# Optimization experiments

Measured on AMD Instinct MI355X. Metric: run time of the kernel, lower is better.

Reference implementation:

```python
import jax, jax.numpy as jnp
import numpy as np

N = 20000      # points
K = 16         # neighbor pairs per query per branch
M = N * K      # total pairs
C = 384        # embed_dim
H = 6          # num_heads
HD = C // H    # head_dim = 64
H1 = H // 2    # cartesian-branch heads
L = 24         # quant_grid_length (window 6.0 / quant 0.25)
Q = 0.25       # quant_size
LS = 24        # quant_grid_length_sphere (120 / 5)
QS = 5.0       # quant_size_sphere
A = 0.05 * 0.25  # exponential_split 'a'
SCALE = HD ** -0.5


def setup_inputs() -> dict:
    key = jax.random.key(0)
    ks = jax.random.split(key, 12)
    s = 0.02
    inp = {}
    inp["query_feats"] = jax.random.normal(ks[0], (N, C), jnp.float32)
    inp["xyz"] = jax.random.uniform(ks[1], (N, 3), jnp.float32, -3.0, 3.0)
    inp["index_0"] = jnp.repeat(jnp.arange(N, dtype=jnp.int32), K)
    inp["index_1"] = jax.random.randint(ks[2], (M,), 0, N, dtype=jnp.int32)
    inp["index_0_sphere"] = jnp.repeat(jnp.arange(N, dtype=jnp.int32), K)
    inp["index_1_sphere"] = jax.random.randint(ks[3], (M,), 0, N, dtype=jnp.int32)
    inp["W_qkv"] = jax.random.normal(ks[4], (C, 3 * C), jnp.float32) * s
    inp["b_qkv"] = jnp.zeros((3 * C,), jnp.float32)
    inp["W_proj"] = jax.random.normal(ks[5], (C, C), jnp.float32) * s
    inp["b_proj"] = jnp.zeros((C,), jnp.float32)
    inp["tq"] = jax.random.normal(ks[6], (2 * L - 1, 3, H1, HD), jnp.float32) * s
    inp["tk"] = jax.random.normal(ks[7], (2 * L - 1, 3, H1, HD), jnp.float32) * s
    inp["tv"] = jax.random.normal(ks[8], (2 * L - 1, 3, H1, HD), jnp.float32) * s
    inp["tq_s"] = jax.random.normal(ks[9], (2 * LS, 3, H - H1, HD), jnp.float32) * s
    inp["tk_s"] = jax.random.normal(ks[10], (2 * LS, 3, H - H1, HD), jnp.float32) * s
    inp["tv_s"] = jax.random.normal(ks[11], (2 * LS, 3, H - H1, HD), jnp.float32) * s
    return inp


def _cart2sphere(xyz):
    x, y, z = xyz[:, 0], xyz[:, 1], xyz[:, 2]
    theta = (jnp.arctan2(y, x) + np.pi) * (180.0 / np.pi)
    beta = jnp.arctan2(jnp.sqrt(x * x + y * y), z) * (180.0 / np.pi)
    r = jnp.sqrt(x * x + y * y + z * z)
    return jnp.stack([theta, beta, r], -1)


def _rel_idx_cart(xyz, i0, i1):
    rel = xyz[i0] - xyz[i1]  # [M,3]
    idx = jnp.floor(rel / Q).astype(jnp.int32) + (L - 1)
    return jnp.clip(idx, 0, 2 * L - 2)


def _rel_idx_sphere(sph, i0, i1):
    rel = sph[i0] - sph[i1]  # [M,3] (theta, beta, r)
    idx01 = jnp.clip(jnp.floor(rel[:, :2] / QS).astype(jnp.int32) + LS, 0, 2 * LS - 1)
    # exponential_split on radial dim
    r = rel[:, 2]
    ra = jnp.abs(r)
    flag = (r >= 0).astype(jnp.float32)
    idx = 2.0 * jnp.floor(jnp.log((ra + 2.0 * A) / A) / np.log(2.0)) - 2.0
    idx = idx + ((3.0 * jnp.exp2(jnp.floor(idx / 2.0)) - 2.0) * A <= ra).astype(jnp.float32)
    idx = idx * (2.0 * flag - 1.0) + (flag - 1.0)
    idx2 = jnp.clip(idx.astype(jnp.int32) + 24, 0, 2 * LS - 1)
    return jnp.concatenate([idx01, idx2[:, None]], 1)


def _branch(q, k, v, i0, i1, rel_idx, Tq, Tk, Tv):
    # q,k,v: [N,h,d]; i0/i1: [M]; rel_idx: [M,3]; tables: [R,3,h,d]
    qg = q[i0]  # [M,h,d]
    kg = k[i1]
    attn = jnp.einsum('mhd,mhd->mh', qg, kg)
    for dim in range(3):
        attn = attn + jnp.einsum('mhd,mhd->mh', qg, Tq[rel_idx[:, dim], dim])
        attn = attn + jnp.einsum('mhd,mhd->mh', kg, Tk[rel_idx[:, dim], dim])
    # segment softmax over queries (i0)
    seg_max = jax.ops.segment_max(attn, i0, num_segments=N)
    ex = jnp.exp(attn - seg_max[i0])
    p = ex / jax.ops.segment_sum(ex, i0, num_segments=N)[i0]  # [M,h]
    vg = v[i1] + Tv[rel_idx[:, 0], 0] + Tv[rel_idx[:, 1], 1] + Tv[rel_idx[:, 2], 2]
    return jax.ops.segment_sum(p[:, :, None] * vg, i0, num_segments=N)  # [N,h,d]


def reference(query_feats, xyz, index_0, index_1, index_0_sphere, index_1_sphere,
              W_qkv, b_qkv, W_proj, b_proj, tq, tk, tv, tq_s, tk_s, tv_s):
    i0 = index_0.astype(jnp.int32)
    i1 = index_1.astype(jnp.int32)
    i0s = index_0_sphere.astype(jnp.int32)
    i1s = index_1_sphere.astype(jnp.int32)
    qkv = (query_feats @ W_qkv + b_qkv).reshape(N, 3, H, HD)
    q = qkv[:, 0] * SCALE
    k = qkv[:, 1]
    v = qkv[:, 2]
    sph = _cart2sphere(xyz)
    ri = _rel_idx_cart(xyz, i0, i1)
    out1 = _branch(q[:, :H1], k[:, :H1], v[:, :H1], i0, i1, ri, tq, tk, tv)
    ri_s = _rel_idx_sphere(sph, i0s, i1s)
    out2 = _branch(q[:, H1:], k[:, H1:], v[:, H1:], i0s, i1s, ri_s, tq_s, tk_s, tv_s)
    x = jnp.concatenate([out1, out2], 1).reshape(N, C)
    return x @ W_proj + b_proj
```

## Files before the change

kernel.cpp:

```cpp
#include <hip/hip_runtime.h>
#include <hip/hip_bf16.h>

namespace {

constexpr int NP   = 20000;
constexpr int CD   = 384;
constexpr int QKVD = 1152;
constexpr int TC   = 47 * 3 * 3 * 64;
constexpr int TS   = 48 * 3 * 3 * 64;

constexpr int PB0 = NP * CD / 4 / 256;
constexpr int PB1 = PB0 + (QKVD / 32) * (CD / 32);
constexpr int PB2 = PB1 + (CD / 32) * (CD / 32);
constexpr int PB3 = PB2 + 27 * 7;

typedef __attribute__((ext_vector_type(8))) short short8;
typedef __attribute__((ext_vector_type(4))) float f32x4;
typedef __attribute__((ext_vector_type(2))) float f32x2;

__device__ inline float f32_atan2(float y, float x) {
  return (float)atan2((double)y, (double)x);
}
__device__ inline float f32_log(float x) {
  return (float)log((double)x);
}

__device__ inline float bfl(unsigned u) {
  union { unsigned u; float f; } c; c.u = u << 16; return c.f;
}
__device__ inline float bfh(unsigned u) {
  union { unsigned u; float f; } c; c.u = u & 0xffff0000u; return c.f;
}
__device__ inline f32x2 up2(unsigned u) {
  f32x2 r;
  r.x = bfl(u);
  r.y = bfh(u);
  return r;
}
__device__ inline unsigned short f2bf(float x) {
  __hip_bfloat16 hb = __float2bfloat16(x);
  unsigned short u; __builtin_memcpy(&u, &hb, 2);
  return u;
}

#if __has_builtin(__builtin_amdgcn_fdot2_f32_bf16)
#define HAVE_BF16_DOT 1
typedef __attribute__((ext_vector_type(2))) __bf16 bf16x2_t;
__device__ inline float dot2bf(unsigned a, unsigned b, float c) {
  bf16x2_t av, bv;
  __builtin_memcpy(&av, &a, 4);
  __builtin_memcpy(&bv, &b, 4);
  return __builtin_amdgcn_fdot2_f32_bf16(av, bv, c, false);
}
#endif

__device__ inline void async16(const void* g, void* l) {
  __builtin_amdgcn_global_load_lds(
      (const __attribute__((address_space(1))) unsigned int*)g,
      (__attribute__((address_space(3))) unsigned int*)l,
      16, 0, 0);
}

__global__ __launch_bounds__(256) void prep_all_k(const float* __restrict__ qf,
                                                  unsigned short* __restrict__ qf_b,
                                                  const float* __restrict__ Wqkv,
                                                  unsigned short* __restrict__ wqkvT,
                                                  const float* __restrict__ Wproj,
                                                  unsigned short* __restrict__ wprojT,
                                                  const float* __restrict__ tq,
                                                  const float* __restrict__ tk,
                                                  const float* __restrict__ tv,
                                                  const float* __restrict__ tqs,
                                                  const float* __restrict__ tks,
                                                  const float* __restrict__ tvs,
                                                  unsigned short* __restrict__ tq_b,
                                                  unsigned short* __restrict__ tk_b,
                                                  unsigned short* __restrict__ tv_b,
                                                  unsigned short* __restrict__ tqs_b,
                                                  unsigned short* __restrict__ tks_b,
                                                  unsigned short* __restrict__ tvs_b,
                                                  const float* __restrict__ xyz,
                                                  float* __restrict__ sph) {
  const int bid = blockIdx.x;
  const int tid = threadIdx.x;
  __shared__ float t[32][33];

  if (bid < PB0) {
    int i = (bid * 256 + tid) * 4;
    float4 v = *(const float4*)(qf + i);
    ushort4 o;
    o.x = f2bf(v.x); o.y = f2bf(v.y); o.z = f2bf(v.z); o.w = f2bf(v.w);
    *(ushort4*)(qf_b + i) = o;
  } else if (bid < PB2) {
    const float* in;
    unsigned short* out;
    int R, Cc, bx, by;
    if (bid < PB1) {
      in = Wqkv; out = wqkvT; R = CD; Cc = QKVD;
      int tt = bid - PB0; bx = tt % (QKVD / 32); by = tt / (QKVD / 32);
    } else {
      in = Wproj; out = wprojT; R = CD; Cc = CD;
      int tt = bid - PB1; bx = tt % (CD / 32); by = tt / (CD / 32);
    }
    const int c0 = bx * 32, r0 = by * 32;
    const int tx = tid & 31, ty = tid >> 5;
    #pragma unroll
    for (int i = 0; i < 32; i += 8)
      t[ty + i][tx] = in[(size_t)(r0 + ty + i) * Cc + (c0 + tx)];
    __syncthreads();
    #pragma unroll
    for (int i = 0; i < 32; i += 8)
      out[(size_t)(c0 + ty + i) * R + (r0 + tx)] = f2bf(t[tx][ty + i]);
  } else {
    const int tt = bid - PB2;
    const int bx = tt % 27, y = tt / 27;
    const int th = bx * 256 + tid;
    if (y < 6) {
      const float* in = (y == 0) ? tq : (y == 1) ? tk : (y == 2) ? tv
                      : (y == 3) ? tqs : (y == 4) ? tks : tvs;
      unsigned short* out = (y == 0) ? tq_b : (y == 1) ? tk_b : (y == 2) ? tv_b
                          : (y == 3) ? tqs_b : (y == 4) ? tks_b : tvs_b;
      const int n = (y < 3) ? TC : TS;
      int i = th * 4;
      if (i < n) {
        float4 v = *(const float4*)(in + i);
        ushort4 o;
        o.x = f2bf(v.x); o.y = f2bf(v.y); o.z = f2bf(v.z); o.w = f2bf(v.w);
        *(ushort4*)(out + i) = o;
      }
    } else {
#pragma clang fp contract(off)
      #pragma unroll
      for (int r = 0; r < 4; ++r) {
        int i = th * 4 + r;
        if (i < NP) {
          const float PIF = 3.14159265358979323846f;
          const float R2D = 57.29577951308232f;
          float x = xyz[i * 3 + 0], yy = xyz[i * 3 + 1], z = xyz[i * 3 + 2];
          float sxy = x * x + yy * yy;
          sph[i * 3 + 0] = (f32_atan2(yy, x) + PIF) * R2D;
          sph[i * 3 + 1] = f32_atan2(sqrtf(sxy), z) * R2D;
          sph[i * 3 + 2] = sqrtf(sxy + z * z);
        }
      }
    }
  }
}

template <int MODE>
__global__ __launch_bounds__(256) void gemm_async_k(const short* __restrict__ A,
                                                    const short* __restrict__ BT,
                                                    const float* __restrict__ bias,
                                                    void* __restrict__ Cout,
                                                    int M, int Nn, int K) {
  __shared__ short As[2][128][32];
  __shared__ short Bs[2][128][32];
  const int tid  = threadIdx.x;
  const int m0   = blockIdx.x * 128, n0 = blockIdx.y * 128;
  const int wave = tid >> 6, lane = tid & 63;
  const int wm   = (wave & 1) * 64, wn = (wave >> 1) * 64;
  const int quad = lane >> 4, l16 = lane & 15;
  const int srow = lane >> 2;
  const int scol = (lane & 3) * 8;

  f32x4 acc[4][4] = {};

  auto stage = [&](int buf, int k0) {
    #pragma unroll
    for (int c = 0; c < 2; ++c) {
      const int base = (wave + c * 4) * 16;
      async16(A + (size_t)(m0 + base + srow) * K + k0 + scol, &As[buf][base][0]);
      async16(BT + (size_t)(n0 + base + srow) * K + k0 + scol, &Bs[buf][base][0]);
    }
  };

  stage(0, 0);
  int cur = 0;
  for (int k0 = 0; k0 < K; k0 += 32) {
    if (k0 + 32 < K) {
      stage(cur ^ 1, k0 + 32);
      asm volatile("s_waitcnt vmcnt(4)" ::: "memory");
    } else {
      asm volatile("s_waitcnt vmcnt(0)" ::: "memory");
    }
    __builtin_amdgcn_s_barrier();
    short8 af[4], bg[4];
    #pragma unroll
    for (int i = 0; i < 4; ++i) af[i] = *(const short8*)&As[cur][wm + i * 16 + l16][quad * 8];
    #pragma unroll
    for (int j = 0; j < 4; ++j) bg[j] = *(const short8*)&Bs[cur][wn + j * 16 + l16][quad * 8];
    #pragma unroll
    for (int i = 0; i < 4; ++i)
      #pragma unroll
      for (int j = 0; j < 4; ++j)
        acc[i][j] = __builtin_amdgcn_mfma_f32_16x16x32_bf16(af[i], bg[j], acc[i][j], 0, 0, 0);
    __builtin_amdgcn_s_barrier();
    cur ^= 1;
  }

  #pragma unroll
  for (int i = 0; i < 4; ++i) {
    #pragma unroll
    for (int j = 0; j < 4; ++j) {
      int gn = n0 + wn + j * 16 + l16;
      if (gn >= Nn) continue;
      float bval = bias[gn];
      #pragma unroll
      for (int r = 0; r < 4; ++r) {
        int gm = m0 + wm + i * 16 + quad * 4 + r;
        if (gm < M) {
          float v = acc[i][j][r] + bval;
          if (MODE == 0) {
            if (gn < 384) v *= 0.125f;
            ((unsigned short*)Cout)[(size_t)gm * Nn + gn] = f2bf(v);
          } else {
            ((float*)Cout)[(size_t)gm * Nn + gn] = v;
          }
        }
      }
    }
  }
}

__device__ inline f32x2 dot8_pk(uint4 q, uint4 k, uint4 a0, uint4 a1, uint4 a2,
                                uint4 t0, uint4 t1, uint4 t2, f32x2 acc) {
  const unsigned* qp = &q.x;  const unsigned* kp = &k.x;
  const unsigned* a0p = &a0.x; const unsigned* a1p = &a1.x; const unsigned* a2p = &a2.x;
  const unsigned* t0p = &t0.x; const unsigned* t1p = &t1.x; const unsigned* t2p = &t2.x;
  #pragma unroll
  for (int w2 = 0; w2 < 4; ++w2) {
    f32x2 qf = up2(qp[w2]), kf = up2(kp[w2]);
    f32x2 tqs = up2(a0p[w2]) + up2(a1p[w2]) + up2(a2p[w2]);
    f32x2 tks = up2(t0p[w2]) + up2(t1p[w2]) + up2(t2p[w2]);
    acc += qf * (kf + tqs) + kf * tks;
  }
  return acc;
}

__device__ inline void acc4(f32x2* vc, uint4 vv, uint4 t0, uint4 t1, uint4 t2,
                            float pr) {
  f32x2 prv = {pr, pr};
  vc[0] += prv * (up2(vv.x) + up2(t0.x) + up2(t1.x) + up2(t2.x));
  vc[1] += prv * (up2(vv.y) + up2(t0.y) + up2(t1.y) + up2(t2.y));
  vc[2] += prv * (up2(vv.z) + up2(t0.z) + up2(t1.z) + up2(t2.z));
  vc[3] += prv * (up2(vv.w) + up2(t0.w) + up2(t1.w) + up2(t2.w));
}

__global__ __launch_bounds__(256, 3) void attn3_k(const unsigned short* __restrict__ qkv,
                                                  const float* __restrict__ xyz,
                                                  const float* __restrict__ sph,
                                                  const int* __restrict__ nb_c,
                                                  const int* __restrict__ nb_s,
                                                  const unsigned short* __restrict__ tq_c,
                                                  const unsigned short* __restrict__ tk_c,
                                                  const unsigned short* __restrict__ tv_c,
                                                  const unsigned short* __restrict__ tq_s,
                                                  const unsigned short* __restrict__ tk_s,
                                                  const unsigned short* __restrict__ tv_s,
                                                  unsigned short* __restrict__ xout) {
  __shared__ int   s_i1 [4][16];
  __shared__ int   s_off[4][16][3];
  __shared__ float s_attn[4][3][16];
  __shared__ float s_p   [4][3][16];

  const int w    = threadIdx.x >> 6;
  const int lane = threadIdx.x & 63;
  const int n    = blockIdx.x * 2 + (w >> 1);
  const int b    = w & 1;

  const unsigned short* tqb = b ? tq_s : tq_c;
  const unsigned short* tkb = b ? tk_s : tk_c;
  const unsigned short* tvb = b ? tv_s : tv_c;

  const int eg = lane >> 2, g = lane & 3;
  const int goff = g * 16;
  const unsigned short* qp = qkv + (size_t)n * QKVD + b * 192 + goff;
  uint4 qv[3][2];
  #pragma unroll
  for (int hh = 0; hh < 3; ++hh) {
    qv[hh][0] = *(const uint4*)(qp + hh * 64);
    qv[hh][1] = *(const uint4*)(qp + hh * 64 + 8);
  }

  if (lane < 16) {
#pragma clang fp contract(off)
    const int e = lane;
    if (b == 0) {
      const int i1 = nb_c[n * 16 + e];
      s_i1[w][e] = i1;
      const float rel[3] = {xyz[n * 3 + 0] - xyz[i1 * 3 + 0],
                            xyz[n * 3 + 1] - xyz[i1 * 3 + 1],
                            xyz[n * 3 + 2] - xyz[i1 * 3 + 2]};
      #pragma unroll
      for (int dim = 0; dim < 3; ++dim) {
        int idx = (int)floorf(rel[dim] * 4.0f) + 23;
        idx = min(max(idx, 0), 46);
        s_off[w][e][dim] = (idx * 3 + dim) * 192;
      }
    } else {
      const int i1 = nb_s[n * 16 + e];
      s_i1[w][e] = i1;
      const float d0 = sph[n * 3 + 0] - sph[i1 * 3 + 0];
      const float d1 = sph[n * 3 + 1] - sph[i1 * 3 + 1];
      const float dr = sph[n * 3 + 2] - sph[i1 * 3 + 2];
      int i0a = (int)floorf(d0 / 5.0f) + 24;
      int i1a = (int)floorf(d1 / 5.0f) + 24;
      const float ra = fabsf(dr);
      const float flag = (dr >= 0.0f) ? 1.0f : 0.0f;
      const float t = (ra + 0.025f) / 0.0125f;
      const float wv = f32_log(t) / 0.69314718055994531f;
      float fidx = 2.0f * floorf(wv) - 2.0f;
      fidx += ((3.0f * exp2f(floorf(fidx * 0.5f)) - 2.0f) * 0.0125f <= ra) ? 1.0f : 0.0f;
      fidx = fidx * (2.0f * flag - 1.0f) + (flag - 1.0f);
      int i2a = (int)fidx + 24;
      s_off[w][e][0] = (min(max(i0a, 0), 47) * 3 + 0) * 192;
      s_off[w][e][1] = (min(max(i1a, 0), 47) * 3 + 1) * 192;
      s_off[w][e][2] = (min(max(i2a, 0), 47) * 3 + 2) * 192;
    }
  }

  {
    const int i1 = s_i1[w][eg];
    const int o0 = s_off[w][eg][0] + goff;
    const int o1 = s_off[w][eg][1] + goff;
    const int o2 = s_off[w][eg][2] + goff;
    const unsigned short* kp = qkv + (size_t)i1 * QKVD + 384 + b * 192 + goff;

    uint4 kc[2][2], ta[2][6], tb[2][6];
#define LDH(buf, ho) do {                                                    \
    kc[buf][0] = *(const uint4*)(kp + (ho));                                 \
    kc[buf][1] = *(const uint4*)(kp + (ho) + 8);                             \
    ta[buf][0] = *(const uint4*)(tqb + o0 + (ho));                           \
    ta[buf][1] = *(const uint4*)(tqb + o0 + (ho) + 8);                       \
    ta[buf][2] = *(const uint4*)(tqb + o1 + (ho));                           \
    ta[buf][3] = *(const uint4*)(tqb + o1 + (ho) + 8);                       \
    ta[buf][4] = *(const uint4*)(tqb + o2 + (ho));                           \
    ta[buf][5] = *(const uint4*)(tqb + o2 + (ho) + 8);                       \
    tb[buf][0] = *(const uint4*)(tkb + o0 + (ho));                           \
    tb[buf][1] = *(const uint4*)(tkb + o0 + (ho) + 8);                       \
    tb[buf][2] = *(const uint4*)(tkb + o1 + (ho));                           \
    tb[buf][3] = *(const uint4*)(tkb + o1 + (ho) + 8);                       \
    tb[buf][4] = *(const uint4*)(tkb + o2 + (ho));                           \
    tb[buf][5] = *(const uint4*)(tkb + o2 + (ho) + 8);                       \
  } while (0)

    LDH(0, 0);
    #pragma unroll
    for (int hh = 0; hh < 3; ++hh) {
      const int cur = hh & 1;
      if (hh < 2) LDH(cur ^ 1, (hh + 1) * 64);
      __builtin_amdgcn_sched_barrier(0);
      float acc;
#ifdef HAVE_BF16_DOT
      float aqk = 0.0f, aq0 = 0.0f, aq1 = 0.0f, aq2 = 0.0f;
      float ak0 = 0.0f, ak1 = 0.0f, ak2 = 0.0f;
      #pragma unroll
      for (int u = 0; u < 2; ++u) {
        const unsigned* qd = (const unsigned*)&qv[hh][u];
        const unsigned* kd = (const unsigned*)&kc[cur][u];
        const unsigned* a0 = (const unsigned*)&ta[cur][u];
        const unsigned* a1 = (const unsigned*)&ta[cur][2 + u];
        const unsigned* a2 = (const unsigned*)&ta[cur][4 + u];
        const unsigned* b0 = (const unsigned*)&tb[cur][u];
        const unsigned* b1 = (const unsigned*)&tb[cur][2 + u];
        const unsigned* b2 = (const unsigned*)&tb[cur][4 + u];
        #pragma unroll
        for (int d = 0; d < 4; ++d) {
          aqk = dot2bf(qd[d], kd[d], aqk);
          aq0 = dot2bf(qd[d], a0[d], aq0);
          aq1 = dot2bf(qd[d], a1[d], aq1);
          aq2 = dot2bf(qd[d], a2[d], aq2);
          ak0 = dot2bf(kd[d], b0[d], ak0);
          ak1 = dot2bf(kd[d], b1[d], ak1);
          ak2 = dot2bf(kd[d], b2[d], ak2);
        }
      }
      acc = ((aqk + aq0) + (aq1 + aq2)) + ((ak0 + ak1) + ak2);
#else
      f32x2 acc2 = {0.0f, 0.0f};
      acc2 = dot8_pk(qv[hh][0], kc[cur][0], ta[cur][0], ta[cur][2], ta[cur][4],
                     tb[cur][0], tb[cur][2], tb[cur][4], acc2);
      acc2 = dot8_pk(qv[hh][1], kc[cur][1], ta[cur][1], ta[cur][3], ta[cur][5],
                     tb[cur][1], tb[cur][3], tb[cur][5], acc2);
      acc = acc2.x + acc2.y;
#endif
      acc += __shfl_xor(acc, 1);
      acc += __shfl_xor(acc, 2);
      if (g == 0) s_attn[w][hh][eg] = acc;
    }
#undef LDH
  }

  if (lane < 48) {
    const int hh = lane >> 4, ee = lane & 15;
    float a = s_attn[w][hh][ee];
    float m = a;
    #pragma unroll
    for (int off = 8; off > 0; off >>= 1) m = fmaxf(m, __shfl_xor(m, off));
    float ex = __expf(a - m);
    float s = ex;
    #pragma unroll
    for (int off = 8; off > 0; off >>= 1) s += __shfl_xor(s, off);
    s_p[w][hh][ee] = ex / s;
  }

  {
    const int e8 = lane >> 3;
    const int c  = lane & 7;
    const int offVa = s_i1[w][e8]     * QKVD + 768 + b * 192 + c * 8;
    const int offVb = s_i1[w][e8 + 8] * QKVD + 768 + b * 192 + c * 8;
    const int offA0 = s_off[w][e8][0] + c * 8;
    const int offA1 = s_off[w][e8][1] + c * 8;
    const int offA2 = s_off[w][e8][2] + c * 8;
    const int offB0 = s_off[w][e8 + 8][0] + c * 8;
    const int offB1 = s_off[w][e8 + 8][1] + c * 8;
    const int offB2 = s_off[w][e8 + 8][2] + c * 8;

    uint4 vA[2], tA0[2], tA1[2], tA2[2], vB[2], tB0[2], tB1[2], tB2[2];
#define LDV(buf, ho) do {                                                    \
    vA [buf] = *(const uint4*)(qkv + offVa + (ho));                          \
    tA0[buf] = *(const uint4*)(tvb + offA0 + (ho));                          \
    tA1[buf] = *(const uint4*)(tvb + offA1 + (ho));                          \
    tA2[buf] = *(const uint4*)(tvb + offA2 + (ho));                          \
    vB [buf] = *(const uint4*)(qkv + offVb + (ho));                          \
    tB0[buf] = *(const uint4*)(tvb + offB0 + (ho));                          \
    tB1[buf] = *(const uint4*)(tvb + offB1 + (ho));                          \
    tB2[buf] = *(const uint4*)(tvb + offB2 + (ho));                          \
  } while (0)

    LDV(0, 0);
    #pragma unroll
    for (int hh = 0; hh < 3; ++hh) {
      const int cur = hh & 1;
      if (hh < 2) LDV(cur ^ 1, (hh + 1) * 64);
      __builtin_amdgcn_sched_barrier(0);
      f32x2 vc[4] = {{0.f, 0.f}, {0.f, 0.f}, {0.f, 0.f}, {0.f, 0.f}};
      acc4(vc, vA[cur], tA0[cur], tA1[cur], tA2[cur], s_p[w][hh][e8]);
      acc4(vc, vB[cur], tB0[cur], tB1[cur], tB2[cur], s_p[w][hh][e8 + 8]);
      #pragma unroll
      for (int q4 = 0; q4 < 4; ++q4) {
        #pragma unroll
        for (int off = 8; off <= 32; off <<= 1) {
          vc[q4].x += __shfl_xor(vc[q4].x, off);
          vc[q4].y += __shfl_xor(vc[q4].y, off);
        }
      }
      if (e8 == 0) {
        uint4 o;
        o.x = ((unsigned)f2bf(vc[0].y) << 16) | (unsigned)f2bf(vc[0].x);
        o.y = ((unsigned)f2bf(vc[1].y) << 16) | (unsigned)f2bf(vc[1].x);
        o.z = ((unsigned)f2bf(vc[2].y) << 16) | (unsigned)f2bf(vc[2].x);
        o.w = ((unsigned)f2bf(vc[3].y) << 16) | (unsigned)f2bf(vc[3].x);
        *(uint4*)(xout + (size_t)n * CD + (b * 3 + hh) * 64 + c * 8) = o;
      }
    }
#undef LDV
  }
}

}

extern "C" void kernel_launch(void* const* d_in, const int* in_sizes, int n_in,
                              void* d_out, int out_size, void* d_ws, size_t ws_size,
                              hipStream_t stream) {
  const float* qf    = (const float*)d_in[0];
  const float* xyz   = (const float*)d_in[1];
  const int*   i1c   = (const int*)d_in[3];
  const int*   i1s   = (const int*)d_in[5];
  const float* Wqkv  = (const float*)d_in[6];
  const float* bqkv  = (const float*)d_in[7];
  const float* Wproj = (const float*)d_in[8];
  const float* bproj = (const float*)d_in[9];
  const float* tq    = (const float*)d_in[10];
  const float* tk    = (const float*)d_in[11];
  const float* tv    = (const float*)d_in[12];
  const float* tqs   = (const float*)d_in[13];
  const float* tks   = (const float*)d_in[14];
  const float* tvs   = (const float*)d_in[15];

  char* w = (char*)d_ws;
  unsigned short* qf_b   = (unsigned short*)w; w += (size_t)NP * CD * 2;
  unsigned short* wqkvT  = (unsigned short*)w; w += (size_t)QKVD * CD * 2;
  unsigned short* wprojT = (unsigned short*)w; w += (size_t)CD * CD * 2;
  unsigned short* qkv_b  = (unsigned short*)w; w += (size_t)NP * QKVD * 2;
  unsigned short* x_b    = (unsigned short*)w; w += (size_t)NP * CD * 2;
  float*          sph    = (float*)w;          w += (size_t)NP * 3 * 4;
  unsigned short* tq_b   = (unsigned short*)w; w += (size_t)TC * 2;
  unsigned short* tk_b   = (unsigned short*)w; w += (size_t)TC * 2;
  unsigned short* tv_b   = (unsigned short*)w; w += (size_t)TC * 2;
  unsigned short* tqs_b  = (unsigned short*)w; w += (size_t)TS * 2;
  unsigned short* tks_b  = (unsigned short*)w; w += (size_t)TS * 2;
  unsigned short* tvs_b  = (unsigned short*)w;

  prep_all_k<<<PB3, 256, 0, stream>>>(qf, qf_b, Wqkv, wqkvT, Wproj, wprojT,
                                      tq, tk, tv, tqs, tks, tvs,
                                      tq_b, tk_b, tv_b, tqs_b, tks_b, tvs_b,
                                      xyz, sph);

  gemm_async_k<0><<<dim3((NP + 127) / 128, QKVD / 128), 256, 0, stream>>>(
      (const short*)qf_b, (const short*)wqkvT, bqkv, qkv_b, NP, QKVD, CD);

  attn3_k<<<NP / 2, 256, 0, stream>>>(qkv_b, xyz, sph, i1c, i1s,
                                      tq_b, tk_b, tv_b, tqs_b, tks_b, tvs_b, x_b);

  gemm_async_k<1><<<dim3((NP + 127) / 128, CD / 128), 256, 0, stream>>>(
      (const short*)x_b, (const short*)wprojT, bproj, d_out, NP, CD, CD);
}
```

Measured before the change: 313.1 us.

## Split attention work to one wavefront per head, one query per block

The attention kernel changes from a block of four waves (two queries, each wave looping over three heads with double-buffered loads) to a 384-thread block per query, where each of six waves handles one head. The softmax is computed in-register with wider shuffles instead of through shared memory, and neighbor index/offset computation is shared per branch behind a __syncthreads. This exposes more parallel waves and fewer registers per wave for latency hiding. In exchange it adds block-level synchronization and loses the explicit software pipelining across heads.

```diff
diff --git a/kernel.cpp b/kernel.cpp
--- a/kernel.cpp
+++ b/kernel.cpp
@@ -246,7 +246,7 @@
   vc[3] += prv * (up2(vv.w) + up2(t0.w) + up2(t1.w) + up2(t2.w));
 }
 
-__global__ __launch_bounds__(256, 3) void attn3_k(const unsigned short* __restrict__ qkv,
+__global__ __launch_bounds__(384, 5) void attn6_k(const unsigned short* __restrict__ qkv,
                                                   const float* __restrict__ xyz,
                                                   const float* __restrict__ sph,
                                                   const int* __restrict__ nb_c,
@@ -258,15 +258,15 @@
                                                   const unsigned short* __restrict__ tk_s,
                                                   const unsigned short* __restrict__ tv_s,
                                                   unsigned short* __restrict__ xout) {
-  __shared__ int   s_i1 [4][16];
-  __shared__ int   s_off[4][16][3];
-  __shared__ float s_attn[4][3][16];
-  __shared__ float s_p   [4][3][16];
+  __shared__ int   s_i1 [2][16];
+  __shared__ int   s_off[2][16][3];
+  __shared__ float s_p  [6][16];
 
   const int w    = threadIdx.x >> 6;
   const int lane = threadIdx.x & 63;
-  const int n    = blockIdx.x * 2 + (w >> 1);
-  const int b    = w & 1;
+  const int n    = blockIdx.x;
+  const int b    = (w >= 3) ? 1 : 0;
+  const int hh   = w - b * 3;
 
   const unsigned short* tqb = b ? tq_s : tq_c;
   const unsigned short* tkb = b ? tk_s : tk_c;
@@ -274,20 +274,16 @@
 
   const int eg = lane >> 2, g = lane & 3;
   const int goff = g * 16;
-  const unsigned short* qp = qkv + (size_t)n * QKVD + b * 192 + goff;
-  uint4 qv[3][2];
-  #pragma unroll
-  for (int hh = 0; hh < 3; ++hh) {
-    qv[hh][0] = *(const uint4*)(qp + hh * 64);
-    qv[hh][1] = *(const uint4*)(qp + hh * 64 + 8);
-  }
-
-  if (lane < 16) {
+  const unsigned short* qp = qkv + (size_t)n * QKVD + b * 192 + hh * 64 + goff;
+  const uint4 qv0 = *(const uint4*)(qp);
+  const uint4 qv1 = *(const uint4*)(qp + 8);
+
+  if (lane < 16 && (w == 0 || w == 3)) {
 #pragma clang fp contract(off)
     const int e = lane;
     if (b == 0) {
       const int i1 = nb_c[n * 16 + e];
-      s_i1[w][e] = i1;
+      s_i1[0][e] = i1;
       const float rel[3] = {xyz[n * 3 + 0] - xyz[i1 * 3 + 0],
                             xyz[n * 3 + 1] - xyz[i1 * 3 + 1],
                             xyz[n * 3 + 2] - xyz[i1 * 3 + 2]};
@@ -295,11 +291,11 @@
       for (int dim = 0; dim < 3; ++dim) {
         int idx = (int)floorf(rel[dim] * 4.0f) + 23;
         idx = min(max(idx, 0), 46);
-        s_off[w][e][dim] = (idx * 3 + dim) * 192;
+        s_off[0][e][dim] = (idx * 3 + dim) * 192;
       }
     } else {
       const int i1 = nb_s[n * 16 + e];
-      s_i1[w][e] = i1;
+      s_i1[1][e] = i1;
       const float d0 = sph[n * 3 + 0] - sph[i1 * 3 + 0];
       const float d1 = sph[n * 3 + 1] - sph[i1 * 3 + 1];
       const float dr = sph[n * 3 + 2] - sph[i1 * 3 + 2];
@@ -313,148 +309,115 @@
       fidx += ((3.0f * exp2f(floorf(fidx * 0.5f)) - 2.0f) * 0.0125f <= ra) ? 1.0f : 0.0f;
       fidx = fidx * (2.0f * flag - 1.0f) + (flag - 1.0f);
       int i2a = (int)fidx + 24;
-      s_off[w][e][0] = (min(max(i0a, 0), 47) * 3 + 0) * 192;
-      s_off[w][e][1] = (min(max(i1a, 0), 47) * 3 + 1) * 192;
-      s_off[w][e][2] = (min(max(i2a, 0), 47) * 3 + 2) * 192;
-    }
-  }
-
+      s_off[1][e][0] = (min(max(i0a, 0), 47) * 3 + 0) * 192;
+      s_off[1][e][1] = (min(max(i1a, 0), 47) * 3 + 1) * 192;
+      s_off[1][e][2] = (min(max(i2a, 0), 47) * 3 + 2) * 192;
+    }
+  }
+  __syncthreads();
+
+  float p;
   {
-    const int i1 = s_i1[w][eg];
-    const int o0 = s_off[w][eg][0] + goff;
-    const int o1 = s_off[w][eg][1] + goff;
-    const int o2 = s_off[w][eg][2] + goff;
-    const unsigned short* kp = qkv + (size_t)i1 * QKVD + 384 + b * 192 + goff;
-
-    uint4 kc[2][2], ta[2][6], tb[2][6];
-#define LDH(buf, ho) do {                                                    \
-    kc[buf][0] = *(const uint4*)(kp + (ho));                                 \
-    kc[buf][1] = *(const uint4*)(kp + (ho) + 8);                             \
-    ta[buf][0] = *(const uint4*)(tqb + o0 + (ho));                           \
-    ta[buf][1] = *(const uint4*)(tqb + o0 + (ho) + 8);                       \
-    ta[buf][2] = *(const uint4*)(tqb + o1 + (ho));                           \
-    ta[buf][3] = *(const uint4*)(tqb + o1 + (ho) + 8);                       \
-    ta[buf][4] = *(const uint4*)(tqb + o2 + (ho));                           \
-    ta[buf][5] = *(const uint4*)(tqb + o2 + (ho) + 8);                       \
-    tb[buf][0] = *(const uint4*)(tkb + o0 + (ho));                           \
-    tb[buf][1] = *(const uint4*)(tkb + o0 + (ho) + 8);                       \
-    tb[buf][2] = *(const uint4*)(tkb + o1 + (ho));                           \
-    tb[buf][3] = *(const uint4*)(tkb + o1 + (ho) + 8);                       \
-    tb[buf][4] = *(const uint4*)(tkb + o2 + (ho));                           \
-    tb[buf][5] = *(const uint4*)(tkb + o2 + (ho) + 8);                       \
-  } while (0)
-
-    LDH(0, 0);
-    #pragma unroll
-    for (int hh = 0; hh < 3; ++hh) {
-      const int cur = hh & 1;
-      if (hh < 2) LDH(cur ^ 1, (hh + 1) * 64);
-      __builtin_amdgcn_sched_barrier(0);
-      float acc;
+    const int i1 = s_i1[b][eg];
+    const int o0 = s_off[b][eg][0] + hh * 64 + goff;
+    const int o1 = s_off[b][eg][1] + hh * 64 + goff;
+    const int o2 = s_off[b][eg][2] + hh * 64 + goff;
+    const unsigned short* kp = qkv + (size_t)i1 * QKVD + 384 + b * 192 + hh * 64 + goff;
+    uint4 kv0 = *(const uint4*)(kp);
+    uint4 kv1 = *(const uint4*)(kp + 8);
+    uint4 a00 = *(const uint4*)(tqb + o0);
+    uint4 a01 = *(const uint4*)(tqb + o0 + 8);
+    uint4 a10 = *(const uint4*)(tqb + o1);
+    uint4 a11 = *(const uint4*)(tqb + o1 + 8);
+    uint4 a20 = *(const uint4*)(tqb + o2);
+    uint4 a21 = *(const uint4*)(tqb + o2 + 8);
+    uint4 b00 = *(const uint4*)(tkb + o0);
+    uint4 b01 = *(const uint4*)(tkb + o0 + 8);
+    uint4 b10 = *(const uint4*)(tkb + o1);
+    uint4 b11 = *(const uint4*)(tkb + o1 + 8);
+    uint4 b20 = *(const uint4*)(tkb + o2);
+    uint4 b21 = *(const uint4*)(tkb + o2 + 8);
+    float acc;
 #ifdef HAVE_BF16_DOT
-      float aqk = 0.0f, aq0 = 0.0f, aq1 = 0.0f, aq2 = 0.0f;
-      float ak0 = 0.0f, ak1 = 0.0f, ak2 = 0.0f;
-      #pragma unroll
-      for (int u = 0; u < 2; ++u) {
-        const unsigned* qd = (const unsigned*)&qv[hh][u];
-        const unsigned* kd = (const unsigned*)&kc[cur][u];
-        const unsigned* a0 = (const unsigned*)&ta[cur][u];
-        const unsigned* a1 = (const unsigned*)&ta[cur][2 + u];
-        const unsigned* a2 = (const unsigned*)&ta[cur][4 + u];
-        const unsigned* b0 = (const unsigned*)&tb[cur][u];
-        const unsigned* b1 = (const unsigned*)&tb[cur][2 + u];
-        const unsigned* b2 = (const unsigned*)&tb[cur][4 + u];
-        #pragma unroll
-        for (int d = 0; d < 4; ++d) {
-          aqk = dot2bf(qd[d], kd[d], aqk);
-          aq0 = dot2bf(qd[d], a0[d], aq0);
-          aq1 = dot2bf(qd[d], a1[d], aq1);
-          aq2 = dot2bf(qd[d], a2[d], aq2);
-          ak0 = dot2bf(kd[d], b0[d], ak0);
-          ak1 = dot2bf(kd[d], b1[d], ak1);
-          ak2 = dot2bf(kd[d], b2[d], ak2);
-        }
-      }
-      acc = ((aqk + aq0) + (aq1 + aq2)) + ((ak0 + ak1) + ak2);
+    float aqk = 0.0f, aq0 = 0.0f, aq1 = 0.0f, aq2 = 0.0f;
+    float ak0 = 0.0f, ak1 = 0.0f, ak2 = 0.0f;
+#define DOT7(qd, kd, a0d, a1d, a2d, b0d, b1d, b2d)                         \
+    aqk = dot2bf(qd, kd, aqk);  aq0 = dot2bf(qd, a0d, aq0);                \
+    aq1 = dot2bf(qd, a1d, aq1); aq2 = dot2bf(qd, a2d, aq2);                \
+    ak0 = dot2bf(kd, b0d, ak0); ak1 = dot2bf(kd, b1d, ak1);                \
+    ak2 = dot2bf(kd, b2d, ak2);
+    DOT7(qv0.x, kv0.x, a00.x, a10.x, a20.x, b00.x, b10.x, b20.x)
+    DOT7(qv0.y, kv0.y, a00.y, a10.y, a20.y, b00.y, b10.y, b20.y)
+    DOT7(qv0.z, kv0.z, a00.z, a10.z, a20.z, b00.z, b10.z, b20.z)
+    DOT7(qv0.w, kv0.w, a00.w, a10.w, a20.w, b00.w, b10.w, b20.w)
+    DOT7(qv1.x, kv1.x, a01.x, a11.x, a21.x, b01.x, b11.x, b21.x)
+    DOT7(qv1.y, kv1.y, a01.y, a11.y, a21.y, b01.y, b11.y, b21.y)
+    DOT7(qv1.z, kv1.z, a01.z, a11.z, a21.z, b01.z, b11.z, b21.z)
+    DOT7(qv1.w, kv1.w, a01.w, a11.w, a21.w, b01.w, b11.w, b21.w)
+#undef DOT7
+    acc = ((aqk + aq0) + (aq1 + aq2)) + ((ak0 + ak1) + ak2);
 #else
-      f32x2 acc2 = {0.0f, 0.0f};
-      acc2 = dot8_pk(qv[hh][0], kc[cur][0], ta[cur][0], ta[cur][2], ta[cur][4],
-                     tb[cur][0], tb[cur][2], tb[cur][4], acc2);
-      acc2 = dot8_pk(qv[hh][1], kc[cur][1], ta[cur][1], ta[cur][3], ta[cur][5],
-                     tb[cur][1], tb[cur][3], tb[cur][5], acc2);
-      acc = acc2.x + acc2.y;
+    f32x2 acc2 = {0.0f, 0.0f};
+    acc2 = dot8_pk(qv0, kv0, a00, a10, a20, b00, b10, b20, acc2);
+    acc2 = dot8_pk(qv1, kv1, a01, a11, a21, b01, b11, b21, acc2);
+    acc = acc2.x + acc2.y;
 #endif
-      acc += __shfl_xor(acc, 1);
-      acc += __shfl_xor(acc, 2);
-      if (g == 0) s_attn[w][hh][eg] = acc;
-    }
-#undef LDH
-  }
-
-  if (lane < 48) {
-    const int hh = lane >> 4, ee = lane & 15;
-    float a = s_attn[w][hh][ee];
-    float m = a;
-    #pragma unroll
-    for (int off = 8; off > 0; off >>= 1) m = fmaxf(m, __shfl_xor(m, off));
-    float ex = __expf(a - m);
+    acc += __shfl_xor(acc, 1);
+    acc += __shfl_xor(acc, 2);
+
+    float m = acc;
+    #pragma unroll
+    for (int off = 4; off <= 32; off <<= 1) m = fmaxf(m, __shfl_xor(m, off));
+    float ex = __expf(acc - m);
     float s = ex;
     #pragma unroll
-    for (int off = 8; off > 0; off >>= 1) s += __shfl_xor(s, off);
-    s_p[w][hh][ee] = ex / s;
+    for (int off = 4; off <= 32; off <<= 1) s += __shfl_xor(s, off);
+    p = ex / s;
+    if (g == 0) s_p[w][eg] = p;
   }
 
   {
     const int e8 = lane >> 3;
     const int c  = lane & 7;
-    const int offVa = s_i1[w][e8]     * QKVD + 768 + b * 192 + c * 8;
-    const int offVb = s_i1[w][e8 + 8] * QKVD + 768 + b * 192 + c * 8;
-    const int offA0 = s_off[w][e8][0] + c * 8;
-    const int offA1 = s_off[w][e8][1] + c * 8;
-    const int offA2 = s_off[w][e8][2] + c * 8;
-    const int offB0 = s_off[w][e8 + 8][0] + c * 8;
-    const int offB1 = s_off[w][e8 + 8][1] + c * 8;
-    const int offB2 = s_off[w][e8 + 8][2] + c * 8;
-
-    uint4 vA[2], tA0[2], tA1[2], tA2[2], vB[2], tB0[2], tB1[2], tB2[2];
-#define LDV(buf, ho) do {                                                    \
-    vA [buf] = *(const uint4*)(qkv + offVa + (ho));                          \
-    tA0[buf] = *(const uint4*)(tvb + offA0 + (ho));                          \
-    tA1[buf] = *(const uint4*)(tvb + offA1 + (ho));                          \
-    tA2[buf] = *(const uint4*)(tvb + offA2 + (ho));                          \
-    vB [buf] = *(const uint4*)(qkv + offVb + (ho));                          \
-    tB0[buf] = *(const uint4*)(tvb + offB0 + (ho));                          \
-    tB1[buf] = *(const uint4*)(tvb + offB1 + (ho));                          \
-    tB2[buf] = *(const uint4*)(tvb + offB2 + (ho));                          \
-  } while (0)
-
-    LDV(0, 0);
-    #pragma unroll
-    for (int hh = 0; hh < 3; ++hh) {
-      const int cur = hh & 1;
-      if (hh < 2) LDV(cur ^ 1, (hh + 1) * 64);
-      __builtin_amdgcn_sched_barrier(0);
-      f32x2 vc[4] = {{0.f, 0.f}, {0.f, 0.f}, {0.f, 0.f}, {0.f, 0.f}};
-      acc4(vc, vA[cur], tA0[cur], tA1[cur], tA2[cur], s_p[w][hh][e8]);
-      acc4(vc, vB[cur], tB0[cur], tB1[cur], tB2[cur], s_p[w][hh][e8 + 8]);
+    const int hc = hh * 64 + c * 8;
+    const int offVa = s_i1[b][e8]     * QKVD + 768 + b * 192 + hc;
+    const int offVb = s_i1[b][e8 + 8] * QKVD + 768 + b * 192 + hc;
+    const int offA0 = s_off[b][e8][0] + hc;
+    const int offA1 = s_off[b][e8][1] + hc;
+    const int offA2 = s_off[b][e8][2] + hc;
+    const int offB0 = s_off[b][e8 + 8][0] + hc;
+    const int offB1 = s_off[b][e8 + 8][1] + hc;
+    const int offB2 = s_off[b][e8 + 8][2] + hc;
+
+    uint4 vA  = *(const uint4*)(qkv + offVa);
+    uint4 tA0 = *(const uint4*)(tvb + offA0);
+    uint4 tA1 = *(const uint4*)(tvb + offA1);
+    uint4 tA2 = *(const uint4*)(tvb + offA2);
+    uint4 vB  = *(const uint4*)(qkv + offVb);
+    uint4 tB0 = *(const uint4*)(tvb + offB0);
+    uint4 tB1 = *(const uint4*)(tvb + offB1);
+    uint4 tB2 = *(const uint4*)(tvb + offB2);
+
+    f32x2 vc[4] = {{0.f, 0.f}, {0.f, 0.f}, {0.f, 0.f}, {0.f, 0.f}};
+    acc4(vc, vA, tA0, tA1, tA2, s_p[w][e8]);
+    acc4(vc, vB, tB0, tB1, tB2, s_p[w][e8 + 8]);
+
+    #pragma unroll
+    for (int q4 = 0; q4 < 4; ++q4) {
       #pragma unroll
-      for (int q4 = 0; q4 < 4; ++q4) {
-        #pragma unroll
-        for (int off = 8; off <= 32; off <<= 1) {
-          vc[q4].x += __shfl_xor(vc[q4].x, off);
-          vc[q4].y += __shfl_xor(vc[q4].y, off);
-        }
+      for (int off = 8; off <= 32; off <<= 1) {
+        vc[q4].x += __shfl_xor(vc[q4].x, off);
+        vc[q4].y += __shfl_xor(vc[q4].y, off);
       }
-      if (e8 == 0) {
-        uint4 o;
-        o.x = ((unsigned)f2bf(vc[0].y) << 16) | (unsigned)f2bf(vc[0].x);
-        o.y = ((unsigned)f2bf(vc[1].y) << 16) | (unsigned)f2bf(vc[1].x);
-        o.z = ((unsigned)f2bf(vc[2].y) << 16) | (unsigned)f2bf(vc[2].x);
-        o.w = ((unsigned)f2bf(vc[3].y) << 16) | (unsigned)f2bf(vc[3].x);
-        *(uint4*)(xout + (size_t)n * CD + (b * 3 + hh) * 64 + c * 8) = o;
-      }
-    }
-#undef LDV
+    }
+    if (e8 == 0) {
+      uint4 o;
+      o.x = ((unsigned)f2bf(vc[0].y) << 16) | (unsigned)f2bf(vc[0].x);
+      o.y = ((unsigned)f2bf(vc[1].y) << 16) | (unsigned)f2bf(vc[1].x);
+      o.z = ((unsigned)f2bf(vc[2].y) << 16) | (unsigned)f2bf(vc[2].x);
+      o.w = ((unsigned)f2bf(vc[3].y) << 16) | (unsigned)f2bf(vc[3].x);
+      *(uint4*)(xout + (size_t)n * CD + (b * 3 + hh) * 64 + c * 8) = o;
+    }
   }
 }
 
@@ -500,8 +463,8 @@
   gemm_async_k<0><<<dim3((NP + 127) / 128, QKVD / 128), 256, 0, stream>>>(
       (const short*)qf_b, (const short*)wqkvT, bqkv, qkv_b, NP, QKVD, CD);
 
-  attn3_k<<<NP / 2, 256, 0, stream>>>(qkv_b, xyz, sph, i1c, i1s,
-                                      tq_b, tk_b, tv_b, tqs_b, tks_b, tvs_b, x_b);
+  attn6_k<<<NP, 384, 0, stream>>>(qkv_b, xyz, sph, i1c, i1s,
+                                  tq_b, tk_b, tv_b, tqs_b, tks_b, tvs_b, x_b);
 
   gemm_async_k<1><<<dim3((NP + 127) / 128, CD / 128), 256, 0, stream>>>(
       (const short*)x_b, (const short*)wprojT, bproj, d_out, NP, CD, CD);
```

After: 325.6 us. 4.0% more time.
